# Optimization experiments

Hardware: AMD Instinct MI355X
Metric: run time of the kernel (lower is better)

The kernel has to match this reference:

```python
import jax, jax.numpy as jnp
import numpy as np
from jax import lax

EPS = 1e-5

def _rsign(x, beta):
    # per-channel learnable shift followed by sign binarization
    return jnp.sign(x + beta[None, :, None, None])

def _scaled_sign_conv(x, w, stride, pad):
    # XNOR-style binarized weights: sign(W) * mean(|W|) per output filter
    alpha = jnp.mean(jnp.abs(w), axis=(1, 2, 3), keepdims=True)
    wb = jnp.sign(w) * alpha
    return lax.conv_general_dilated(x, wb, (stride, stride), [(pad, pad), (pad, pad)],
                                    dimension_numbers=('NCHW', 'OIHW', 'NCHW'))

def _bn(x, gamma, beta):
    # training-mode batch norm (batch statistics), matching torch default forward
    m = jnp.mean(x, axis=(0, 2, 3), keepdims=True)
    v = jnp.var(x, axis=(0, 2, 3), keepdims=True)
    xn = (x - m) * lax.rsqrt(v + EPS)
    return xn * gamma[None, :, None, None] + beta[None, :, None, None]

def _rprelu(x, gamma, zeta, slope):
    g = gamma[None, :, None, None]
    s = slope[None, :, None, None]
    xs = x - g
    return jnp.where(xs > 0, xs, s * xs) + zeta[None, :, None, None]

def _avgpool2(x):
    B, C, H, W = x.shape
    return x.reshape(B, C, H // 2, 2, W // 2, 2).mean(axis=(3, 5))

def reference(x, rsign1_beta, w1, bn1_gamma, bn1_beta, rsign2_beta, w2, bn2_gamma, bn2_beta, pr_gamma, pr_zeta, pr_slope):
    # layer1: RSign -> 3x3 stride-2 scaled_sign conv -> BN
    out1 = _bn(_scaled_sign_conv(_rsign(x, rsign1_beta), w1, 2, 1), bn1_gamma, bn1_beta)
    out1 = out1 + _avgpool2(x)
    out1 = _rprelu(out1, pr_gamma, pr_zeta, pr_slope)
    # layer2 (shared weights, called twice with identical inputs -> identical outputs)
    out2 = _bn(_scaled_sign_conv(_rsign(out1, rsign2_beta), w2, 1, 0), bn2_gamma, bn2_beta)
    y = out2 + out1
    return jnp.concatenate([y, y], axis=1)

def setup_inputs() -> dict:
    key = jax.random.key(0)
    ks = jax.random.split(key, 8)
    B, C, H, W = 32, 256, 56, 56
    return {
        'x': jax.random.normal(ks[0], (B, C, H, W), jnp.float32),
        'rsign1_beta': jax.random.normal(ks[1], (C,), jnp.float32) * 0.1,
        'w1': jax.random.normal(ks[2], (C, C, 3, 3), jnp.float32) * 0.05,
        'bn1_gamma': jnp.ones((C,), jnp.float32),
        'bn1_beta': jnp.zeros((C,), jnp.float32),
        'rsign2_beta': jax.random.normal(ks[3], (C,), jnp.float32) * 0.1,
        'w2': jax.random.normal(ks[4], (C, C, 1, 1), jnp.float32) * 0.05,
        'bn2_gamma': jnp.ones((C,), jnp.float32),
        'bn2_beta': jnp.zeros((C,), jnp.float32),
        'pr_gamma': jax.random.normal(ks[5], (C,), jnp.float32) * 0.1,
        'pr_zeta': jax.random.normal(ks[6], (C,), jnp.float32) * 0.1,
        'pr_slope': jnp.full((C,), 0.25, jnp.float32),
    }
```

## Files before the change

### kernel.cpp

```cpp
#include <hip/hip_runtime.h>
#include <stdint.h>

typedef unsigned long long u64;
typedef uint32_t u32;

#define BB  32
#define CC  256
#define HH  56
#define WW  56
#define OHH 28
#define OWW 28
#define NPIX (BB*OHH*OWW)

__global__ __launch_bounds__(256) void rrb_prep_w(const float* __restrict__ w1,
                                                  const float* __restrict__ w2,
                                                  u32* __restrict__ wp1, u32* __restrict__ wp2,
                                                  float* __restrict__ alpha1, float* __restrict__ alpha2) {
    __shared__ float red[256];
    int co = blockIdx.x & 255;
    int t = threadIdx.x;
    int wid = t >> 6, lane = t & 63;
    float asum = 0.f;
    if (blockIdx.x < 256) {
        const float* wr = w1 + (size_t)co * 2304 + (size_t)t * 9;
        float v[9];
        #pragma unroll
        for (int k = 0; k < 9; ++k) { v[k] = wr[k]; asum += fabsf(v[k]); }
        #pragma unroll
        for (int k = 0; k < 9; ++k) {
            u64 m = __ballot(v[k] > 0.f);
            if (lane == 0)
                *(u64*)&wp1[((size_t)co * 9 + k) * 8 + 2 * wid] = m;
        }
    } else {
        float v = w2[co * 256 + t];
        asum = fabsf(v);
        u64 m = __ballot(v > 0.f);
        if (lane == 0) *(u64*)&wp2[co * 8 + 2 * wid] = m;
    }
    red[t] = asum; __syncthreads();
    for (int st = 128; st > 0; st >>= 1) {
        if (t < st) red[t] += red[t + st];
        __syncthreads();
    }
    if (t == 0) {
        if (blockIdx.x < 256) alpha1[co] = red[0] / 2304.f;
        else                  alpha2[co] = red[0] / 256.f;
    }
}

__global__ __launch_bounds__(256) void rrb_pack_x(const float* __restrict__ x,
                                                  const float* __restrict__ rsb1,
                                                  u32* __restrict__ xb, float* __restrict__ pool) {
    int i = blockIdx.x * 256 + threadIdx.x;
    int s  = i & 3;
    int i2 = i >> 2;
    int ow = i2 % OWW;
    int i3 = i2 / OWW;
    int oh = i3 % OHH;
    int i4 = i3 / OHH;
    int n  = i4 & 31;
    int j  = i4 >> 5;
    int c0 = 32 * j + 8 * s;
    const float* base = x + (((size_t)(n * CC + c0) * HH + 2 * oh) * WW + 2 * ow);

    float2 a0[8], a1[8];
    #pragma unroll
    for (int cc = 0; cc < 8; ++cc) {
        const float* p = base + (size_t)cc * (HH * WW);
        a0[cc] = *(const float2*)p;
        a1[cc] = *(const float2*)(p + WW);
    }
    float4 b0 = *(const float4*)&rsb1[c0];
    float4 b1 = *(const float4*)&rsb1[c0 + 4];

    u32 w00 = 0, w01 = 0, w10 = 0, w11 = 0;
    float pv[8];
    #pragma unroll
    for (int cc = 0; cc < 8; ++cc) {
        float b = (cc < 4) ? ((const float*)&b0)[cc] : ((const float*)&b1)[cc - 4];
        w00 |= (u32)(a0[cc].x + b > 0.f) << cc;
        w01 |= (u32)(a0[cc].y + b > 0.f) << cc;
        w10 |= (u32)(a1[cc].x + b > 0.f) << cc;
        w11 |= (u32)(a1[cc].y + b > 0.f) << cc;
        pv[cc] = (a0[cc].x + a0[cc].y + a1[cc].x + a1[cc].y) * 0.25f;
    }
    w00 <<= 8 * s; w01 <<= 8 * s; w10 <<= 8 * s; w11 <<= 8 * s;
    w00 |= __shfl_xor(w00, 1); w00 |= __shfl_xor(w00, 2);
    w01 |= __shfl_xor(w01, 1); w01 |= __shfl_xor(w01, 2);
    w10 |= __shfl_xor(w10, 1); w10 |= __shfl_xor(w10, 2);
    w11 |= __shfl_xor(w11, 1); w11 |= __shfl_xor(w11, 2);

    float* pp = pool + ((size_t)(n * OHH + oh) * OWW + ow) * CC + c0;
    *(float4*)&pp[0] = make_float4(pv[0], pv[1], pv[2], pv[3]);
    *(float4*)&pp[4] = make_float4(pv[4], pv[5], pv[6], pv[7]);

    u32* xo = xb + (((size_t)(n * HH + 2 * oh) * WW + 2 * ow) * 8) + j;
    u32 wsel = (s == 0) ? w00 : (s == 1) ? w01 : (s == 2) ? w10 : w11;
    int off = (s == 0) ? 0 : (s == 1) ? 8 : (s == 2) ? WW * 8 : WW * 8 + 8;
    xo[off] = wsel;
}

__global__ __launch_bounds__(256) void rrb_conv1(const u32* __restrict__ xb,
                                                 const u32* __restrict__ wp1,
                                                 short* __restrict__ S1,
                                                 int* __restrict__ s_sum, u64* __restrict__ s_sq) {
    __shared__ u32 xs[3 * WW * 8];
    int blk = blockIdx.x;
    int n = blk / OHH, oh = blk - n * OHH;
    int t = threadIdx.x;
    int r0 = 2 * oh - 1;
    for (int i = t; i < 3 * WW * 8; i += 256) {
        int row = i / (WW * 8);
        int ih = r0 + row;
        xs[i] = (ih >= 0) ? xb[((size_t)(n * HH + ih) * WW) * 8 + (i - row * WW * 8)] : 0u;
    }
    u32 wreg[72];
    {
        const u32* wsrc = wp1 + (size_t)t * 72;
        #pragma unroll
        for (int i = 0; i < 72; ++i) wreg[i] = wsrc[i];
    }
    __syncthreads();
    bool oh0 = (oh == 0);
    int bsum = 0; long long bsq = 0;
    short* outp = S1 + ((size_t)(n * OHH + oh) * OWW) * CC + t;
    for (int ow = 0; ow < OWW; ++ow) {
        int S = 0;
        #pragma unroll
        for (int kh = 0; kh < 3; ++kh) {
            bool vkh = !(kh == 0 && oh0);
            #pragma unroll
            for (int kw = 0; kw < 3; ++kw) {
                int iw = 2 * ow + kw - 1;
                bool ok = vkh && (iw >= 0);
                int iwc = iw < 0 ? 0 : iw;
                const u32* xp = &xs[(kh * WW + iwc) * 8];
                int p = 0;
                #pragma unroll
                for (int j = 0; j < 8; ++j) p += __popc(xp[j] ^ wreg[(kh * 3 + kw) * 8 + j]);
                S += ok ? (256 - 2 * p) : 0;
            }
        }
        outp[ow * CC] = (short)S;
        bsum += S;
        bsq += (long long)S * S;
    }
    atomicAdd(&s_sum[t], bsum);
    atomicAdd(&s_sq[t], (u64)bsq);
}

__global__ void rrb_finalize(const int* __restrict__ ssum, const u64* __restrict__ ssq,
                             const float* __restrict__ alpha,
                             const float* __restrict__ gamma, const float* __restrict__ beta,
                             float* __restrict__ A, float* __restrict__ Bv) {
    int c = threadIdx.x;
    const double N = (double)NPIX;
    double s = (double)ssum[c];
    double q = (double)ssq[c];
    double mS = s / N;
    double vS = q / N - mS * mS;
    double al = (double)alpha[c];
    double mean = al * mS;
    double var = al * al * vS;
    double scale = (double)gamma[c] / sqrt(var + 1e-5);
    A[c] = (float)(al * scale);
    Bv[c] = (float)((double)beta[c] - mean * scale);
}

__global__ __launch_bounds__(256) void rrb_out1(const short* __restrict__ S1,
                                                float* __restrict__ pool,
                                                const float* __restrict__ A1, const float* __restrict__ B1,
                                                const float* __restrict__ pg, const float* __restrict__ pz,
                                                const float* __restrict__ ps, const float* __restrict__ rsb2,
                                                u32* __restrict__ x2b) {
    int blk = blockIdx.x;
    int half = blk & 1;
    int rest = blk >> 1;
    int n = rest / OHH, oh = rest - n * OHH;
    int owlo = half * 14;
    int c = threadIdx.x;
    int wid = c >> 6, lane = c & 63;
    float a = A1[c], b = B1[c];
    float g = pg[c], z = pz[c], s = ps[c], b2 = rsb2[c];
    size_t pixbase = ((size_t)(n * OHH + oh) * OWW + owlo);
    const short* sp = S1 + pixbase * CC + c;
    float* pp = pool + pixbase * CC + c;
    u32* xo = x2b + pixbase * 8;
    float sv[14], pv[14];
    #pragma unroll
    for (int k = 0; k < 14; ++k) sv[k] = (float)sp[k * CC];
    #pragma unroll
    for (int k = 0; k < 14; ++k) pv[k] = pp[k * CC];
    #pragma unroll
    for (int k = 0; k < 14; ++k) {
        float v = a * sv[k] + b + pv[k];
        float xsv = v - g;
        float o = (xsv > 0.f ? xsv : s * xsv) + z;
        pp[k * CC] = o;
        u64 m = __ballot(o + b2 > 0.f);
        if (lane == 0) *(u64*)&xo[k * 8 + 2 * wid] = m;
    }
}

__global__ __launch_bounds__(256) void rrb_conv2(const u32* __restrict__ x2b,
                                                 const u32* __restrict__ wp2,
                                                 short* __restrict__ S2,
                                                 int* __restrict__ s_sum, u64* __restrict__ s_sq) {
    __shared__ u32 xs[14 * 8];
    int blk = blockIdx.x;
    int half = blk & 1;
    int rest = blk >> 1;
    int n = rest / OHH, oh = rest - n * OHH;
    int owlo = half * 14;
    int t = threadIdx.x;
    size_t pixbase = ((size_t)(n * OHH + oh) * OWW + owlo);
    const u32* src = x2b + pixbase * 8;
    if (t < 14 * 8) xs[t] = src[t];
    u32 wr[8];
    {
        const u32* wsv = wp2 + (size_t)t * 8;
        #pragma unroll
        for (int j = 0; j < 8; ++j) wr[j] = wsv[j];
    }
    __syncthreads();
    int bsum = 0; long long bsq = 0;
    short* outp = S2 + pixbase * CC + t;
    #pragma unroll
    for (int ow = 0; ow < 14; ++ow) {
        int p = 0;
        #pragma unroll
        for (int j = 0; j < 8; ++j) p += __popc(xs[ow * 8 + j] ^ wr[j]);
        int S = 256 - 2 * p;
        outp[ow * CC] = (short)S;
        bsum += S;
        bsq += (long long)S * S;
    }
    atomicAdd(&s_sum[t], bsum);
    atomicAdd(&s_sq[t], (u64)bsq);
}

__global__ __launch_bounds__(256) void rrb_final(const short* __restrict__ S2,
                                                 const float* __restrict__ out1,
                                                 const float* __restrict__ A2, const float* __restrict__ B2,
                                                 float* __restrict__ y) {
    int blk = blockIdx.x;
    int half = blk & 1;
    int rest = blk >> 1;
    int n = rest / OHH, oh = rest - n * OHH;
    int owlo = half * 16;
    int cnt = half ? 12 : 16;
    int c = threadIdx.x;
    float a = A2[c], b = B2[c];
    size_t pixbase = ((size_t)(n * OHH + oh) * OWW + owlo);
    const short* sp = S2 + pixbase * CC + c;
    const float* op = out1 + pixbase * CC + c;
    float buf[16];
    if (half) {
        #pragma unroll
        for (int k = 0; k < 12; ++k) buf[k] = a * (float)sp[k * CC] + b + op[k * CC];
    } else {
        #pragma unroll
        for (int k = 0; k < 16; ++k) buf[k] = a * (float)sp[k * CC] + b + op[k * CC];
    }
    float* y0 = y + ((size_t)(n * 2 * CC + c) * OHH + oh) * OWW + owlo;
    float* y1 = y0 + (size_t)CC * OHH * OWW;
    int k4 = cnt / 4;
    for (int k = 0; k < k4; ++k) {
        float4 v = make_float4(buf[4 * k], buf[4 * k + 1], buf[4 * k + 2], buf[4 * k + 3]);
        *(float4*)&y0[4 * k] = v;
        *(float4*)&y1[4 * k] = v;
    }
}

extern "C" void kernel_launch(void* const* d_in, const int* in_sizes, int n_in,
                              void* d_out, int out_size, void* d_ws, size_t ws_size,
                              hipStream_t stream) {
    const float* x    = (const float*)d_in[0];
    const float* rsb1 = (const float*)d_in[1];
    const float* w1   = (const float*)d_in[2];
    const float* bn1g = (const float*)d_in[3];
    const float* bn1b = (const float*)d_in[4];
    const float* rsb2 = (const float*)d_in[5];
    const float* w2   = (const float*)d_in[6];
    const float* bn2g = (const float*)d_in[7];
    const float* bn2b = (const float*)d_in[8];
    const float* pg   = (const float*)d_in[9];
    const float* pz   = (const float*)d_in[10];
    const float* ps   = (const float*)d_in[11];
    float* y = (float*)d_out;

    char* ws = (char*)d_ws;
    if (ws_size < 55488512) return;

    u32*   wp1    = (u32*)(ws + 0);
    u32*   wp2    = (u32*)(ws + 73728);
    float* alpha1 = (float*)(ws + 81920);
    float* alpha2 = (float*)(ws + 82944);
    float* A1     = (float*)(ws + 83968);
    float* B1     = (float*)(ws + 84992);
    float* A2     = (float*)(ws + 86016);
    float* B2     = (float*)(ws + 87040);
    int*   st1_sum = (int*)(ws + 88064);
    u64*   st1_sq  = (u64*)(ws + 89088);
    int*   st2_sum = (int*)(ws + 91136);
    u64*   st2_sq  = (u64*)(ws + 92160);
    u32*   xb   = (u32*)(ws + 94208);
    float* pool = (float*)(ws + 3305472);
    short* S1   = (short*)(ws + 28995584);
    u32*   x2b  = (u32*)(ws + 41840640);
    short* S2   = (short*)(ws + 42643456);

    hipMemsetAsync(ws + 88064, 0, 6144, stream);

    rrb_prep_w<<<512, 256, 0, stream>>>(w1, w2, wp1, wp2, alpha1, alpha2);
    rrb_pack_x<<<(BB * OHH * OWW * 8 * 4) / 256, 256, 0, stream>>>(x, rsb1, xb, pool);
    rrb_conv1<<<BB * OHH, 256, 0, stream>>>(xb, wp1, S1, st1_sum, st1_sq);
    rrb_finalize<<<1, 256, 0, stream>>>(st1_sum, st1_sq, alpha1, bn1g, bn1b, A1, B1);
    rrb_out1<<<BB * OHH * 2, 256, 0, stream>>>(S1, pool, A1, B1, pg, pz, ps, rsb2, x2b);
    rrb_conv2<<<BB * OHH * 2, 256, 0, stream>>>(x2b, wp2, S2, st2_sum, st2_sq);
    rrb_finalize<<<1, 256, 0, stream>>>(st2_sum, st2_sq, alpha2, bn2g, bn2b, A2, B2);
    rrb_final<<<BB * OHH * 2, 256, 0, stream>>>(S2, pool, A2, B2, y);
}
```

Before: 177.1 us.

## Fold BN finalize into consumers, zero stats in prep, transpose final via LDS

Removes the memset and both single-block finalize launches. Stats zeroing moves into the weight-prep kernel, and each consumer kernel computes the BN scale and shift per channel from the accumulated sums. The final kernel now handles a whole output row per block and transposes through shared memory, so NCHW writes come out as coalesced float4 stores instead of strided per-channel writes. The cost is redundant double-precision BN math in every block and a larger LDS footprint in the final kernel, which may lower occupancy.

```diff
diff --git a/kernel.cpp b/kernel.cpp
--- a/kernel.cpp
+++ b/kernel.cpp
@@ -15,11 +15,16 @@
 __global__ __launch_bounds__(256) void rrb_prep_w(const float* __restrict__ w1,
                                                   const float* __restrict__ w2,
                                                   u32* __restrict__ wp1, u32* __restrict__ wp2,
-                                                  float* __restrict__ alpha1, float* __restrict__ alpha2) {
+                                                  float* __restrict__ alpha1, float* __restrict__ alpha2,
+                                                  u32* __restrict__ stats_zero) {
     __shared__ float red[256];
     int co = blockIdx.x & 255;
     int t = threadIdx.x;
     int wid = t >> 6, lane = t & 63;
+    if (blockIdx.x == 0) {
+        #pragma unroll
+        for (int k = 0; k < 6; ++k) stats_zero[k * 256 + t] = 0u;
+    }
     float asum = 0.f;
     if (blockIdx.x < 256) {
         const float* wr = w1 + (size_t)co * 2304 + (size_t)t * 9;
@@ -150,27 +155,25 @@
     atomicAdd(&s_sq[t], (u64)bsq);
 }
 
-__global__ void rrb_finalize(const int* __restrict__ ssum, const u64* __restrict__ ssq,
-                             const float* __restrict__ alpha,
-                             const float* __restrict__ gamma, const float* __restrict__ beta,
-                             float* __restrict__ A, float* __restrict__ Bv) {
-    int c = threadIdx.x;
+__device__ __forceinline__ void bn_fold(const int* ssum, const u64* ssq,
+                                        const float* alpha, const float* gamma,
+                                        const float* beta, int c, float& a, float& b) {
     const double N = (double)NPIX;
     double s = (double)ssum[c];
     double q = (double)ssq[c];
     double mS = s / N;
     double vS = q / N - mS * mS;
     double al = (double)alpha[c];
-    double mean = al * mS;
-    double var = al * al * vS;
-    double scale = (double)gamma[c] / sqrt(var + 1e-5);
-    A[c] = (float)(al * scale);
-    Bv[c] = (float)((double)beta[c] - mean * scale);
+    double scale = (double)gamma[c] / sqrt(al * al * vS + 1e-5);
+    a = (float)(al * scale);
+    b = (float)((double)beta[c] - al * mS * scale);
 }
 
 __global__ __launch_bounds__(256) void rrb_out1(const short* __restrict__ S1,
                                                 float* __restrict__ pool,
-                                                const float* __restrict__ A1, const float* __restrict__ B1,
+                                                const int* __restrict__ ssum, const u64* __restrict__ ssq,
+                                                const float* __restrict__ alpha1,
+                                                const float* __restrict__ bn1g, const float* __restrict__ bn1b,
                                                 const float* __restrict__ pg, const float* __restrict__ pz,
                                                 const float* __restrict__ ps, const float* __restrict__ rsb2,
                                                 u32* __restrict__ x2b) {
@@ -181,7 +184,8 @@
     int owlo = half * 14;
     int c = threadIdx.x;
     int wid = c >> 6, lane = c & 63;
-    float a = A1[c], b = B1[c];
+    float a, b;
+    bn_fold(ssum, ssq, alpha1, bn1g, bn1b, c, a, b);
     float g = pg[c], z = pz[c], s = ps[c], b2 = rsb2[c];
     size_t pixbase = ((size_t)(n * OHH + oh) * OWW + owlo);
     const short* sp = S1 + pixbase * CC + c;
@@ -242,34 +246,32 @@
 
 __global__ __launch_bounds__(256) void rrb_final(const short* __restrict__ S2,
                                                  const float* __restrict__ out1,
-                                                 const float* __restrict__ A2, const float* __restrict__ B2,
+                                                 const int* __restrict__ ssum, const u64* __restrict__ ssq,
+                                                 const float* __restrict__ alpha2,
+                                                 const float* __restrict__ bn2g, const float* __restrict__ bn2b,
                                                  float* __restrict__ y) {
+    __shared__ float lds[256 * 29];
     int blk = blockIdx.x;
-    int half = blk & 1;
-    int rest = blk >> 1;
-    int n = rest / OHH, oh = rest - n * OHH;
-    int owlo = half * 16;
-    int cnt = half ? 12 : 16;
+    int n = blk / OHH, oh = blk - n * OHH;
     int c = threadIdx.x;
-    float a = A2[c], b = B2[c];
-    size_t pixbase = ((size_t)(n * OHH + oh) * OWW + owlo);
+    float a, b;
+    bn_fold(ssum, ssq, alpha2, bn2g, bn2b, c, a, b);
+    size_t pixbase = ((size_t)(n * OHH + oh) * OWW);
     const short* sp = S2 + pixbase * CC + c;
     const float* op = out1 + pixbase * CC + c;
-    float buf[16];
-    if (half) {
-        #pragma unroll
-        for (int k = 0; k < 12; ++k) buf[k] = a * (float)sp[k * CC] + b + op[k * CC];
-    } else {
-        #pragma unroll
-        for (int k = 0; k < 16; ++k) buf[k] = a * (float)sp[k * CC] + b + op[k * CC];
-    }
-    float* y0 = y + ((size_t)(n * 2 * CC + c) * OHH + oh) * OWW + owlo;
-    float* y1 = y0 + (size_t)CC * OHH * OWW;
-    int k4 = cnt / 4;
-    for (int k = 0; k < k4; ++k) {
-        float4 v = make_float4(buf[4 * k], buf[4 * k + 1], buf[4 * k + 2], buf[4 * k + 3]);
-        *(float4*)&y0[4 * k] = v;
-        *(float4*)&y1[4 * k] = v;
+    #pragma unroll
+    for (int ow = 0; ow < OWW; ++ow)
+        lds[c * 29 + ow] = a * (float)sp[ow * CC] + b + op[ow * CC];
+    __syncthreads();
+    #pragma unroll
+    for (int it = 0; it < 7; ++it) {
+        int idx = it * 256 + c;
+        int cp = idx / 7, qq = idx - cp * 7;
+        const float* lp = &lds[cp * 29 + 4 * qq];
+        float4 v = make_float4(lp[0], lp[1], lp[2], lp[3]);
+        float* dst = y + ((size_t)(n * 2 * CC + cp) * OHH + oh) * OWW + 4 * qq;
+        *(float4*)dst = v;
+        *(float4*)(dst + (size_t)CC * OHH * OWW) = v;
     }
 }
 
@@ -297,10 +299,6 @@
     u32*   wp2    = (u32*)(ws + 73728);
     float* alpha1 = (float*)(ws + 81920);
     float* alpha2 = (float*)(ws + 82944);
-    float* A1     = (float*)(ws + 83968);
-    float* B1     = (float*)(ws + 84992);
-    float* A2     = (float*)(ws + 86016);
-    float* B2     = (float*)(ws + 87040);
     int*   st1_sum = (int*)(ws + 88064);
     u64*   st1_sq  = (u64*)(ws + 89088);
     int*   st2_sum = (int*)(ws + 91136);
@@ -311,14 +309,13 @@
     u32*   x2b  = (u32*)(ws + 41840640);
     short* S2   = (short*)(ws + 42643456);
 
-    hipMemsetAsync(ws + 88064, 0, 6144, stream);
-
-    rrb_prep_w<<<512, 256, 0, stream>>>(w1, w2, wp1, wp2, alpha1, alpha2);
+    rrb_prep_w<<<512, 256, 0, stream>>>(w1, w2, wp1, wp2, alpha1, alpha2,
+                                        (u32*)(ws + 88064));
     rrb_pack_x<<<(BB * OHH * OWW * 8 * 4) / 256, 256, 0, stream>>>(x, rsb1, xb, pool);
     rrb_conv1<<<BB * OHH, 256, 0, stream>>>(xb, wp1, S1, st1_sum, st1_sq);
-    rrb_finalize<<<1, 256, 0, stream>>>(st1_sum, st1_sq, alpha1, bn1g, bn1b, A1, B1);
-    rrb_out1<<<BB * OHH * 2, 256, 0, stream>>>(S1, pool, A1, B1, pg, pz, ps, rsb2, x2b);
+    rrb_out1<<<BB * OHH * 2, 256, 0, stream>>>(S1, pool, st1_sum, st1_sq, alpha1,
+                                               bn1g, bn1b, pg, pz, ps, rsb2, x2b);
     rrb_conv2<<<BB * OHH * 2, 256, 0, stream>>>(x2b, wp2, S2, st2_sum, st2_sq);
-    rrb_finalize<<<1, 256, 0, stream>>>(st2_sum, st2_sq, alpha2, bn2g, bn2b, A2, B2);
-    rrb_final<<<BB * OHH * 2, 256, 0, stream>>>(S2, pool, A2, B2, y);
-}
+    rrb_final<<<BB * OHH, 256, 0, stream>>>(S2, pool, st2_sum, st2_sq, alpha2,
+                                            bn2g, bn2b, y);
+}
```

New measurement: 157.6 us. -11.0%, faster.
